# Kernel tuning notes

Hardware: AMD Instinct MI355X
Metric: run time of the kernel (lower is better)

## Reference

```python
import jax, jax.numpy as jnp
import numpy as np

DIM = 512
NUM_HEADS = 8
HEAD_DIM = DIM // NUM_HEADS
SCALE = HEAD_DIM ** -0.5
HIDDEN = int(DIM * 4.0)
LN_EPS = 1e-5


def layer_norm(x, w, b):
    mu = jnp.mean(x, axis=-1, keepdims=True)
    var = jnp.var(x, axis=-1, keepdims=True)
    return (x - mu) * jax.lax.rsqrt(var + LN_EPS) * w + b


def setup_inputs() -> dict:
    key = jax.random.key(0)
    ks = jax.random.split(key, 8)
    s = 0.02
    return {
        "x": jax.random.normal(ks[0], (8, 4096, DIM), dtype=jnp.float32),
        "ln1_w": jnp.ones((DIM,), jnp.float32),
        "ln1_b": jnp.zeros((DIM,), jnp.float32),
        "qkv_w": jax.random.normal(ks[1], (3 * DIM, DIM), jnp.float32) * s,
        "proj_w": jax.random.normal(ks[2], (DIM, DIM), jnp.float32) * s,
        "proj_b": jnp.zeros((DIM,), jnp.float32),
        "ln2_w": jnp.ones((DIM,), jnp.float32),
        "ln2_b": jnp.zeros((DIM,), jnp.float32),
        "fc1_w": jax.random.normal(ks[3], (HIDDEN, DIM), jnp.float32) * s,
        "fc1_b": jnp.zeros((HIDDEN,), jnp.float32),
        "fc2_w": jax.random.normal(ks[4], (DIM, HIDDEN), jnp.float32) * s,
        "fc2_b": jnp.zeros((DIM,), jnp.float32),
        "eca_w": jax.random.normal(ks[5], (1, 1, 3), jnp.float32) * 0.5,
    }


def channel_attention(x, qkv_w, proj_w, proj_b):
    B, N, C = x.shape
    qkv = (x @ qkv_w.T).reshape(B, N, 3, NUM_HEADS, HEAD_DIM)
    qkv = qkv.transpose(2, 0, 3, 1, 4)  # (3, B, h, N, hd)
    q, k, v = qkv[0], qkv[1] * SCALE, qkv[2]
    # cross-covariance attention: (hd x hd) per head
    attn = jax.nn.softmax(jnp.einsum("bhnd,bhne->bhde", k, v), axis=-1)
    out = jnp.einsum("bhde,bhne->bhnd", attn, q)  # (B, h, N, hd)
    out = out.transpose(0, 2, 1, 3).reshape(B, N, C)
    return out @ proj_w.T + proj_b


def mlp_eca(x, fc1_w, fc1_b, fc2_w, fc2_b, eca_w):
    B, N, C = x.shape
    H = W = int(np.sqrt(N))
    h = jax.nn.gelu(x @ fc1_w.T + fc1_b, approximate=False)
    y = h @ fc2_w.T + fc2_b  # (B, N, C)
    # faithful replication of torch .view(B, C, H, W) on contiguous (B, N, C)
    y4 = y.reshape(B, C, H, W)
    pooled = jnp.mean(y4, axis=(2, 3))  # (B, C)
    conv = jax.lax.conv_general_dilated(
        pooled[:, None, :], eca_w, window_strides=(1,), padding=[(1, 1)],
        dimension_numbers=("NCW", "OIW", "NCW"))[:, 0, :]  # (B, C)
    gate = jax.nn.sigmoid(conv)[:, :, None, None]
    y4 = y4 * gate + y4
    return y4.reshape(B, C, H * W).transpose(0, 2, 1)  # (B, N, C)


def reference(x, ln1_w, ln1_b, qkv_w, proj_w, proj_b, ln2_w, ln2_b,
              fc1_w, fc1_b, fc2_w, fc2_b, eca_w):
    cur = layer_norm(x, ln1_w, ln1_b)
    x = x + channel_attention(cur, qkv_w, proj_w, proj_b)
    x = x + mlp_eca(layer_norm(x, ln2_w, ln2_b), fc1_w, fc1_b, fc2_w, fc2_b, eca_w)
    return x
```

## Files before the change

### kernel.cpp

```cpp
#include <hip/hip_runtime.h>
#include <hip/hip_bf16.h>

typedef __bf16 bf16;
typedef __bf16 bf16x8 __attribute__((ext_vector_type(8)));
typedef float floatx4 __attribute__((ext_vector_type(4)));

#define B_    8
#define N_    4096
#define C_    512
#define BN_   32768
#define HID_  2048
#define SCALE_ 0.125f

__device__ __forceinline__ void load_lds16(const void* g, void* l) {
    __builtin_amdgcn_global_load_lds(
        (const __attribute__((address_space(1))) void*)g,
        (__attribute__((address_space(3))) void*)l, 16, 0, 0);
}

__global__ void sniff_kernel(const unsigned int* __restrict__ xw, int* __restrict__ flag)
{
    int t = threadIdx.x;
    int votes = 0;
#pragma unroll
    for (int i = 0; i < 4; i++) {
        unsigned w = xw[t * 4 + i];
        if (w == 0u) continue;
        unsigned a = w & 0xFFFFu;
        unsigned e = (a >> 7) & 0xFFu;
        if (a != 0u && e >= 110u && e <= 135u) votes++; else votes--;
    }
#pragma unroll
    for (int off = 32; off; off >>= 1) votes += __shfl_xor(votes, off);
    __shared__ int s[4];
    if ((t & 63) == 0) s[t >> 6] = votes;
    __syncthreads();
    if (t == 0) *flag = (s[0] + s[1] + s[2] + s[3]) > 0 ? 1 : 0;
}

struct ConvArgs {
    const void* src[12];
    unsigned    dstoff[12];
    int         n[12];
};

__global__ __launch_bounds__(256) void convert_params(
    ConvArgs args, char* __restrict__ ws, const int* __restrict__ flag)
{
    int seg = blockIdx.y;
    int n = args.n[seg];
    int base = blockIdx.x * 2048;
    if (base >= n) return;
    bf16* dst = (bf16*)(ws + args.dstoff[seg]);
    const void* src = args.src[seg];
    bool isbf = (*flag != 0);
#pragma unroll
    for (int j = 0; j < 8; j++) {
        int idx = base + threadIdx.x + j * 256;
        if (idx < n) {
            float v = isbf ? (float)((const bf16*)src)[idx]
                           : ((const float*)src)[idx];
            dst[idx] = (bf16)v;
        }
    }
}

__device__ __forceinline__ void ln_core(float f[8], const bf16* w, const bf16* b,
                                        int lane, bf16* outp)
{
    float s = 0.f, sq = 0.f;
#pragma unroll
    for (int j = 0; j < 8; j++) { s += f[j]; sq += f[j]*f[j]; }
#pragma unroll
    for (int off = 32; off; off >>= 1) { s += __shfl_xor(s, off); sq += __shfl_xor(sq, off); }
    float mean = s * (1.f/512.f);
    float var  = sq * (1.f/512.f) - mean*mean;
    float inv  = rsqrtf(var + 1e-5f);
    bf16x8 wv = *(const bf16x8*)(w + lane*8);
    bf16x8 bv = *(const bf16x8*)(b + lane*8);
    bf16x8 o;
#pragma unroll
    for (int j = 0; j < 8; j++) o[j] = (bf16)((f[j]-mean)*inv*(float)wv[j] + (float)bv[j]);
    *(bf16x8*)outp = o;
}

__global__ __launch_bounds__(256) void ln_dyn_kernel(
    const void* __restrict__ xv, const bf16* __restrict__ w,
    const bf16* __restrict__ b, bf16* __restrict__ out, const int* __restrict__ flag)
{
    int wave = threadIdx.x >> 6, lane = threadIdx.x & 63;
    size_t row = (size_t)blockIdx.x * 4 + wave;
    float f[8];
    if (*flag) {
        bf16x8 v = *(const bf16x8*)((const bf16*)xv + row * C_ + lane * 8);
#pragma unroll
        for (int j = 0; j < 8; j++) f[j] = (float)v[j];
    } else {
        const float4* p = (const float4*)((const float*)xv + row * C_ + lane * 8);
        float4 v0 = p[0], v1 = p[1];
        f[0]=v0.x; f[1]=v0.y; f[2]=v0.z; f[3]=v0.w;
        f[4]=v1.x; f[5]=v1.y; f[6]=v1.z; f[7]=v1.w;
    }
    ln_core(f, w, b, lane, out + row * C_ + lane*8);
}

__global__ __launch_bounds__(256) void ln_b16_kernel(
    const bf16* __restrict__ x, const bf16* __restrict__ w,
    const bf16* __restrict__ b, bf16* __restrict__ out)
{
    int wave = threadIdx.x >> 6, lane = threadIdx.x & 63;
    size_t row = (size_t)blockIdx.x * 4 + wave;
    bf16x8 v = *(const bf16x8*)(x + row * C_ + lane * 8);
    float f[8];
#pragma unroll
    for (int j = 0; j < 8; j++) f[j] = (float)v[j];
    ln_core(f, w, b, lane, out + row * C_ + lane*8);
}

__global__ __launch_bounds__(256) void ln_f32_kernel(
    const float* __restrict__ x, const bf16* __restrict__ w,
    const bf16* __restrict__ b, bf16* __restrict__ out)
{
    int wave = threadIdx.x >> 6, lane = threadIdx.x & 63;
    size_t row = (size_t)blockIdx.x * 4 + wave;
    const float4* p = (const float4*)(x + row * C_ + lane * 8);
    float4 v0 = p[0], v1 = p[1];
    float f[8] = { v0.x, v0.y, v0.z, v0.w, v1.x, v1.y, v1.z, v1.w };
    ln_core(f, w, b, lane, out + row * C_ + lane*8);
}

enum { EPI_NONE = 0, EPI_BIAS = 1, EPI_BIAS_RESID = 2, EPI_BIAS_GELU = 3, EPI_QKV = 4 };

__device__ __forceinline__ void stage_half(
    const bf16* __restrict__ G, int ldk, bf16* lbase, int t)
{
#pragma unroll
    for (int i = 0; i < 2; i++) {
        int c  = i * 512 + t;
        int cp = c ^ (((c >> 5) & 1) << 1);
        load_lds16(G + (size_t)(cp >> 3) * ldk + (cp & 7) * 8, lbase + c * 8);
    }
}

#define PHASE(qq)  {                                                           \
    constexpr int aH = (qq) >> 1, bH = (qq) & 1;                               \
    const bf16* Ab = &Asl[s][aH][0][0];                                        \
    const bf16* Bb = &Bsl[s][bH][0][0];                                        \
    bf16x8 af[4][2], bfv[2][2];                                                \
    _Pragma("unroll") for (int mi = 0; mi < 4; mi++) {                         \
        int row = wm * 64 + mi * 16 + l16;                                     \
        int xo  = ((row >> 2) & 1) << 4;                                       \
        _Pragma("unroll") for (int ks = 0; ks < 2; ks++)                       \
            af[mi][ks] = *(const bf16x8*)(Ab + row * 64 +                      \
                          ((ks * 32 + quad * 8) ^ xo));                        \
    }                                                                          \
    _Pragma("unroll") for (int ni = 0; ni < 2; ni++) {                         \
        int row = wn * 32 + ni * 16 + l16;                                     \
        int xo  = ((row >> 2) & 1) << 4;                                       \
        _Pragma("unroll") for (int ks = 0; ks < 2; ks++)                       \
            bfv[ni][ks] = *(const bf16x8*)(Bb + row * 64 +                     \
                          ((ks * 32 + quad * 8) ^ xo));                        \
    }                                                                          \
    if ((qq) == 0 && kt + 1 < NKT)                                             \
        stage_half(A + (size_t)(m0 + 128) * K + (size_t)(kt + 1) * 64, K,      \
                   &Asl[s ^ 1][1][0][0], t);                                   \
    if ((qq) == 1 && kt + 1 < NKT)                                             \
        stage_half(W + (size_t)(n0 + 128) * K + (size_t)(kt + 1) * 64, K,      \
                   &Bsl[s ^ 1][1][0][0], t);                                   \
    if ((qq) == 2 && kt + 2 < NKT)                                             \
        stage_half(A + (size_t)m0 * K + (size_t)(kt + 2) * 64, K,              \
                   &Asl[s][0][0][0], t);                                       \
    if ((qq) == 3 && kt + 2 < NKT)                                             \
        stage_half(W + (size_t)n0 * K + (size_t)(kt + 2) * 64, K,              \
                   &Bsl[s][0][0][0], t);                                       \
    if ((qq) == 3 && kt + 1 < NKT) {                                           \
        if (kt + 2 < NKT) asm volatile("s_waitcnt vmcnt(4)");                  \
        else              asm volatile("s_waitcnt vmcnt(0)");                  \
    }                                                                          \
    __builtin_amdgcn_s_barrier();                                              \
    asm volatile("s_waitcnt lgkmcnt(0)");                                      \
    __builtin_amdgcn_s_setprio(1);                                             \
    _Pragma("unroll") for (int mi = 0; mi < 4; mi++)                           \
    _Pragma("unroll") for (int ni = 0; ni < 2; ni++)                           \
    _Pragma("unroll") for (int ks = 0; ks < 2; ks++)                           \
        acc[aH * 4 + mi][bH * 2 + ni] = __builtin_amdgcn_mfma_f32_16x16x32_bf16( \
            af[mi][ks], bfv[ni][ks], acc[aH * 4 + mi][bH * 2 + ni], 0, 0, 0);  \
    __builtin_amdgcn_s_setprio(0);                                             \
    __builtin_amdgcn_s_barrier();                                              \
}

template<typename OutT, int EPI>
__global__ __launch_bounds__(512, 2) void gemm256(
    const bf16* __restrict__ A, const bf16* __restrict__ W,
    const bf16* __restrict__ bias, const void* __restrict__ resid,
    const int* __restrict__ flag,
    OutT* __restrict__ Cout, bf16* __restrict__ Cout2, int M, int Nn, int K)
{
    __shared__ bf16 Asl[2][2][128][64];
    __shared__ bf16 Bsl[2][2][128][64];
    const int t = threadIdx.x;
    const int wv = t >> 6, lane = t & 63;
    const int quad = lane >> 4, l16 = lane & 15;
    const int wm = wv >> 2, wn = wv & 3;
    const int Nt = Nn >> 8;
    const int id = blockIdx.x;
    const int xcd = id & 7, j = id >> 3;
    const int m0 = ((j / Nt) * 8 + xcd) * 256;
    const int n0 = (j % Nt) * 256;
    const int NKT = K >> 6;

    floatx4 acc[8][4] = {};

    stage_half(A + (size_t)m0 * K,           K, &Asl[0][0][0][0], t);
    stage_half(W + (size_t)n0 * K,           K, &Bsl[0][0][0][0], t);
    stage_half(A + (size_t)(m0 + 128) * K,   K, &Asl[0][1][0][0], t);
    stage_half(W + (size_t)(n0 + 128) * K,   K, &Bsl[0][1][0][0], t);
    stage_half(A + (size_t)m0 * K + 64,      K, &Asl[1][0][0][0], t);
    stage_half(W + (size_t)n0 * K + 64,      K, &Bsl[1][0][0][0], t);
    asm volatile("s_waitcnt vmcnt(4)");
    __builtin_amdgcn_s_barrier();

    for (int kt = 0; kt < NKT; ++kt) {
        const int s = kt & 1;
        PHASE(0) PHASE(1) PHASE(2) PHASE(3)
    }

    size_t ldc = (size_t)Nn; int csub = 0; bool to2 = false;
    if (EPI == EPI_QKV) {
        if (n0 >= 512) { to2 = true; ldc = 1024; csub = 512; }
        else           { ldc = 512; }
    }
    bool isbf = false;
    if (EPI == EPI_BIAS_RESID) isbf = (*flag != 0);

#pragma unroll
    for (int mg = 0; mg < 8; mg++) {
        int rowg = m0 + (mg >> 2) * 128 + wm * 64 + (mg & 3) * 16 + quad * 4;
#pragma unroll
        for (int ng = 0; ng < 4; ng++) {
            int col = n0 + (ng >> 1) * 128 + wn * 32 + (ng & 1) * 16 + l16;
            float bv = (EPI == EPI_BIAS || EPI == EPI_BIAS_RESID || EPI == EPI_BIAS_GELU)
                       ? (float)bias[col] : 0.f;
#pragma unroll
            for (int r = 0; r < 4; r++) {
                size_t idx = (size_t)(rowg + r) * ldc + (col - csub);
                float v = acc[mg][ng][r] + bv;
                if (EPI == EPI_BIAS_RESID) {
                    float rres = isbf ? (float)((const bf16*)resid)[idx]
                                      : ((const float*)resid)[idx];
                    v += rres;
                }
                if (EPI == EPI_BIAS_GELU)  v = 0.5f * v * (1.f + erff(v * 0.70710678118654752f));
                if (EPI == EPI_QKV && to2) Cout2[idx] = (bf16)v;
                else                       Cout[idx]  = (OutT)v;
            }
        }
    }
}

__global__ __launch_bounds__(256) void attn_logits_mfma(
    const bf16* __restrict__ kv, float* __restrict__ partial)
{
    __shared__ bf16 Kt[64][136];
    __shared__ bf16 Vt[64][136];
    int s = blockIdx.x, bh = blockIdx.y, b = bh >> 3, h = bh & 7;
    int t = threadIdx.x, wave = t >> 6, lane = t & 63;
    int quad = lane >> 4, l16 = lane & 15;
    floatx4 acc[4] = {};
    for (int c = 0; c < 4; c++) {
        int n0 = s * 512 + c * 128;
        {
            int isv = t >> 7;
            int r   = t & 127;
            const bf16* gp = &kv[((size_t)b * N_ + n0 + r) * 1024 + h * 64 + isv * 512];
            bf16x8 rowv[8];
#pragma unroll
            for (int u = 0; u < 8; u++) rowv[u] = *(const bf16x8*)(gp + u * 8);
            bf16 (*dst)[136] = isv ? Vt : Kt;
#pragma unroll
            for (int u = 0; u < 8; u++)
#pragma unroll
                for (int jj = 0; jj < 8; jj++)
                    dst[u * 8 + jj][r] = rowv[u][jj];
        }
        __syncthreads();
#pragma unroll
        for (int ks = 0; ks < 4; ks++) {
            bf16x8 af = *(const bf16x8*)&Kt[wave * 16 + l16][ks * 32 + quad * 8];
#pragma unroll
            for (int ni = 0; ni < 4; ni++) {
                bf16x8 bfv = *(const bf16x8*)&Vt[ni * 16 + l16][ks * 32 + quad * 8];
                acc[ni] = __builtin_amdgcn_mfma_f32_16x16x32_bf16(af, bfv, acc[ni], 0, 0, 0);
            }
        }
        __syncthreads();
    }
    float* p = partial + ((size_t)bh * 8 + s) * 4096;
#pragma unroll
    for (int ni = 0; ni < 4; ni++)
#pragma unroll
        for (int r = 0; r < 4; r++)
            p[(wave * 16 + quad * 4 + r) * 64 + ni * 16 + l16] = acc[ni][r];
}

__global__ __launch_bounds__(256) void attn_softmax_kernel(
    const float* __restrict__ partial, bf16* __restrict__ attnb)
{
    int bh = blockIdx.y;
    int wave = threadIdx.x >> 6, lane = threadIdx.x & 63;
    for (int r = 0; r < 4; r++) {
        int d = blockIdx.x * 16 + wave * 4 + r;
        float v = 0.f;
#pragma unroll
        for (int s = 0; s < 8; s++) v += partial[((size_t)bh*8 + s)*4096 + d*64 + lane];
        v *= SCALE_;
        float m = v;
#pragma unroll
        for (int off = 32; off; off >>= 1) m = fmaxf(m, __shfl_xor(m, off));
        float p = expf(v - m);
        float sum = p;
#pragma unroll
        for (int off = 32; off; off >>= 1) sum += __shfl_xor(sum, off);
        attnb[(size_t)bh*4096 + d*64 + lane] = (bf16)(p / sum);
    }
}

__global__ __launch_bounds__(256) void attn_apply_mfma(
    const bf16* __restrict__ q, const bf16* __restrict__ attnb,
    bf16* __restrict__ outT)
{
    int bh = blockIdx.y, b = bh >> 3, h = bh & 7;
    int t = threadIdx.x, wave = t >> 6, lane = t & 63;
    int quad = lane >> 4, l16 = lane & 15;
    int nbase = blockIdx.x * 256 + wave * 64;
    bf16x8 bfrag[4][2];
#pragma unroll
    for (int di = 0; di < 4; di++)
#pragma unroll
        for (int ks = 0; ks < 2; ks++)
            bfrag[di][ks] = *(const bf16x8*)&attnb[(size_t)bh*4096 + (di*16 + l16)*64 + ks*32 + quad*8];
    floatx4 acc[4][4] = {};
#pragma unroll
    for (int mi = 0; mi < 4; mi++) {
#pragma unroll
        for (int ks = 0; ks < 2; ks++) {
            bf16x8 af = *(const bf16x8*)&q[((size_t)b*N_ + nbase + mi*16 + l16)*512 + h*64 + ks*32 + quad*8];
#pragma unroll
            for (int di = 0; di < 4; di++)
                acc[mi][di] = __builtin_amdgcn_mfma_f32_16x16x32_bf16(af, bfrag[di][ks], acc[mi][di], 0, 0, 0);
        }
    }
#pragma unroll
    for (int mi = 0; mi < 4; mi++)
#pragma unroll
        for (int di = 0; di < 4; di++)
#pragma unroll
            for (int r = 0; r < 4; r++)
                outT[((size_t)b*N_ + nbase + mi*16 + quad*4 + r)*512 + h*64 + di*16 + l16] =
                    (bf16)acc[mi][di][r];
}

__global__ __launch_bounds__(256) void pooled_kernel(
    const bf16* __restrict__ y, float* __restrict__ pooled)
{
    int bc = blockIdx.x;
    const bf16* p = y + (size_t)bc * 4096 + threadIdx.x * 16;
    float s = 0.f;
#pragma unroll
    for (int i = 0; i < 2; i++) {
        bf16x8 v = *(const bf16x8*)(p + i*8);
#pragma unroll
        for (int j = 0; j < 8; j++) s += (float)v[j];
    }
#pragma unroll
    for (int off = 32; off; off >>= 1) s += __shfl_xor(s, off);
    __shared__ float red[4];
    if ((threadIdx.x & 63) == 0) red[threadIdx.x >> 6] = s;
    __syncthreads();
    if (threadIdx.x == 0)
        pooled[bc] = (red[0] + red[1] + red[2] + red[3]) * (1.f/4096.f);
}

__global__ void gate_kernel(const float* __restrict__ pooled,
                            const bf16* __restrict__ eca_w, float* __restrict__ gate1)
{
    int c = threadIdx.x, b = blockIdx.x;
    float w0 = (float)eca_w[0], w1 = (float)eca_w[1], w2 = (float)eca_w[2];
    const float* p = pooled + b * 512;
    float conv = w1 * p[c];
    if (c > 0)   conv += w0 * p[c-1];
    if (c < 511) conv += w2 * p[c+1];
    float g = 1.f / (1.f + expf(-conv));
    gate1[b * 512 + c] = 1.f + g;
}

__global__ __launch_bounds__(256) void final_rmw(
    const bf16* __restrict__ y, const float* __restrict__ gate1,
    float* __restrict__ out)
{
    int b = blockIdx.z, c0 = blockIdx.y * 64, n0 = blockIdx.x * 64;
    __shared__ float ytile[64][65];
    int t = threadIdx.x;
#pragma unroll
    for (int i = 0; i < 2; i++) {
        int chunk = t * 2 + i;
        int ci = chunk >> 3, nj = (chunk & 7) * 8;
        bf16x8 v = *(const bf16x8*)&y[(size_t)b * ((size_t)N_*C_) + (size_t)(c0+ci) * 4096 + n0 + nj];
#pragma unroll
        for (int j = 0; j < 8; j++) ytile[ci][nj+j] = (float)v[j];
    }
    __syncthreads();
    int cc = t & 63, nb = t >> 6;
    float g = gate1[b * 512 + c0 + cc];
    for (int p = 0; p < 16; p++) {
        int nr = p * 4 + nb;
        size_t idx = ((size_t)b * N_ + n0 + nr) * C_ + c0 + cc;
        out[idx] = out[idx] + g * ytile[cc][nr];
    }
}

__global__ __launch_bounds__(256) void final_fresh(
    const bf16* __restrict__ y, const bf16* __restrict__ x2b,
    const float* __restrict__ gate1, float* __restrict__ out)
{
    int b = blockIdx.z, c0 = blockIdx.y * 64, n0 = blockIdx.x * 64;
    __shared__ float ytile[64][65];
    int t = threadIdx.x;
#pragma unroll
    for (int i = 0; i < 2; i++) {
        int chunk = t * 2 + i;
        int ci = chunk >> 3, nj = (chunk & 7) * 8;
        bf16x8 v = *(const bf16x8*)&y[(size_t)b * ((size_t)N_*C_) + (size_t)(c0+ci) * 4096 + n0 + nj];
#pragma unroll
        for (int j = 0; j < 8; j++) ytile[ci][nj+j] = (float)v[j];
    }
    __syncthreads();
    int cc = t & 63, nb = t >> 6;
    float g = gate1[b * 512 + c0 + cc];
    for (int p = 0; p < 16; p++) {
        int nr = p * 4 + nb;
        size_t idx = ((size_t)b * N_ + n0 + nr) * C_ + c0 + cc;
        out[idx] = (float)x2b[idx] + g * ytile[cc][nr];
    }
}

extern "C" void kernel_launch(void* const* d_in, const int* in_sizes, int n_in,
                              void* d_out, int out_size, void* d_ws, size_t ws_size,
                              hipStream_t stream)
{
    float* outf = (float*)d_out;
    bf16*  outb = (bf16*)d_out;
    char* ws = (char*)d_ws;

    int*   flag    = (int*)ws;
    float* pooled  = (float*)(ws + 4096);
    float* gate1   = (float*)(ws + 20480);
    bf16* ln1_w = (bf16*)(ws + 65536);
    bf16* ln1_b = (bf16*)(ws + 67584);
    bf16* ln2_w = (bf16*)(ws + 69632);
    bf16* ln2_b = (bf16*)(ws + 71680);
    bf16* proj_b= (bf16*)(ws + 73728);
    bf16* fc2_b = (bf16*)(ws + 75776);
    bf16* eca_w = (bf16*)(ws + 77824);
    bf16* fc1_b = (bf16*)(ws + 81920);
    bf16* qkv_w = (bf16*)(ws + ((size_t)1 << 20));
    bf16* proj_w= (bf16*)(ws + (size_t)2621440);
    bf16* fc1_w = (bf16*)(ws + ((size_t)3 << 20));
    bf16* fc2_w = (bf16*)(ws + ((size_t)5 << 20));
    float* partial = (float*)(ws + ((size_t)7  << 20));
    bf16*  attnb   = (bf16*)(ws + ((size_t)15 << 20));
    bf16*  T1      = (bf16*)(ws + ((size_t)16 << 20));
    bf16*  kvbuf   = (bf16*)(ws + ((size_t)48 << 20));
    bf16*  hbuf    = kvbuf;
    bf16*  x2b     = (bf16*)(ws + ((size_t)176 << 20));

    const bool fat = ws_size >= ((size_t)212 << 20);

    sniff_kernel<<<1, 256, 0, stream>>>((const unsigned int*)d_in[0], flag);

    ConvArgs ca;
    const int   srcidx[12] = { 1, 2, 6, 7, 5, 11, 12, 9, 3, 4, 8, 10 };
    const unsigned offs[12] = { 65536, 67584, 69632, 71680, 73728, 75776, 77824, 81920,
                                1u<<20, 2621440u, 3u<<20, 5u<<20 };
    for (int i = 0; i < 12; i++) {
        ca.src[i] = d_in[srcidx[i]];
        ca.dstoff[i] = offs[i];
        ca.n[i] = in_sizes[srcidx[i]];
    }
    convert_params<<<dim3(512, 12), 256, 0, stream>>>(ca, ws, flag);

    ln_dyn_kernel<<<BN_/4, 256, 0, stream>>>(d_in[0], ln1_w, ln1_b, T1, flag);

    gemm256<bf16, EPI_QKV><<<768, 512, 0, stream>>>(
        T1, qkv_w, nullptr, nullptr, flag, outb, kvbuf, BN_, 1536, 512);

    attn_logits_mfma<<<dim3(8, 64), 256, 0, stream>>>(kvbuf, partial);
    attn_softmax_kernel<<<dim3(4, 64), 256, 0, stream>>>(partial, attnb);
    attn_apply_mfma<<<dim3(16, 64), 256, 0, stream>>>(outb, attnb, T1);

    if (fat) {
        gemm256<bf16, EPI_BIAS_RESID><<<256, 512, 0, stream>>>(
            T1, proj_w, proj_b, d_in[0], flag, x2b, nullptr, BN_, 512, 512);
        ln_b16_kernel<<<BN_/4, 256, 0, stream>>>(x2b, ln2_w, ln2_b, T1);
        gemm256<bf16, EPI_BIAS_GELU><<<1024, 512, 0, stream>>>(
            T1, fc1_w, fc1_b, nullptr, flag, hbuf, nullptr, BN_, 2048, 512);
        gemm256<bf16, EPI_BIAS><<<256, 512, 0, stream>>>(
            hbuf, fc2_w, fc2_b, nullptr, flag, T1, nullptr, BN_, 512, 2048);
        pooled_kernel<<<4096, 256, 0, stream>>>(T1, pooled);
        gate_kernel<<<8, 512, 0, stream>>>(pooled, eca_w, gate1);
        final_fresh<<<dim3(64, 8, 8), 256, 0, stream>>>(T1, x2b, gate1, outf);
    } else {
        gemm256<float, EPI_BIAS_RESID><<<256, 512, 0, stream>>>(
            T1, proj_w, proj_b, d_in[0], flag, outf, nullptr, BN_, 512, 512);
        ln_f32_kernel<<<BN_/4, 256, 0, stream>>>(outf, ln2_w, ln2_b, T1);
        for (int ch = 0; ch < 2; ch++) {
            bf16* Tch = T1 + (size_t)ch * 16384 * 512;
            gemm256<bf16, EPI_BIAS_GELU><<<512, 512, 0, stream>>>(
                Tch, fc1_w, fc1_b, nullptr, flag, hbuf, nullptr, 16384, 2048, 512);
            gemm256<bf16, EPI_BIAS><<<128, 512, 0, stream>>>(
                hbuf, fc2_w, fc2_b, nullptr, flag, Tch, nullptr, 16384, 512, 2048);
        }
        pooled_kernel<<<4096, 256, 0, stream>>>(T1, pooled);
        gate_kernel<<<8, 512, 0, stream>>>(pooled, eca_w, gate1);
        final_rmw<<<dim3(64, 8, 8), 256, 0, stream>>>(T1, gate1, outf);
    }
}
```

Baseline: 608.2 us.

## Reorder GEMM quadrants to reuse fragments and use full 8-way LDS swizzle

Changes the LDS swizzle in the 256x256 GEMM from a 1-bit XOR to a full 3-bit XOR on the row index, so the 16-byte fragment reads spread across all banks. It also reorders the four MFMA quadrants (00, 01, 11, 10) so A and B register fragments carry over between phases. This cuts LDS reads per k-tile from four A and four B loads to two of each. The cost is more live fragment registers (af, bf0, bf1) under a 512-thread, 2-blocks-per-CU launch bound, which could cause register spills.

```diff
diff --git a/kernel.cpp b/kernel.cpp
--- a/kernel.cpp
+++ b/kernel.cpp
@@ -137,57 +137,37 @@
 #pragma unroll
     for (int i = 0; i < 2; i++) {
         int c  = i * 512 + t;
-        int cp = c ^ (((c >> 5) & 1) << 1);
-        load_lds16(G + (size_t)(cp >> 3) * ldk + (cp & 7) * 8, lbase + c * 8);
-    }
-}
-
-#define PHASE(qq)  {                                                           \
-    constexpr int aH = (qq) >> 1, bH = (qq) & 1;                               \
-    const bf16* Ab = &Asl[s][aH][0][0];                                        \
-    const bf16* Bb = &Bsl[s][bH][0][0];                                        \
-    bf16x8 af[4][2], bfv[2][2];                                                \
+        int r  = c >> 3;
+        int ls = (c & 7) ^ (r & 7);
+        load_lds16(G + (size_t)r * ldk + ls * 8, lbase + c * 8);
+    }
+}
+
+#define LOAD_AF(half)                                                          \
     _Pragma("unroll") for (int mi = 0; mi < 4; mi++) {                         \
         int row = wm * 64 + mi * 16 + l16;                                     \
-        int xo  = ((row >> 2) & 1) << 4;                                       \
         _Pragma("unroll") for (int ks = 0; ks < 2; ks++)                       \
-            af[mi][ks] = *(const bf16x8*)(Ab + row * 64 +                      \
-                          ((ks * 32 + quad * 8) ^ xo));                        \
-    }                                                                          \
+            af[mi][ks] = *(const bf16x8*)(&Asl[s][half][0][0] + row * 64 +     \
+                ((ks * 32 + quad * 8) ^ ((row & 7) << 3)));                    \
+    }
+#define LOAD_BF(dst, half)                                                     \
     _Pragma("unroll") for (int ni = 0; ni < 2; ni++) {                         \
         int row = wn * 32 + ni * 16 + l16;                                     \
-        int xo  = ((row >> 2) & 1) << 4;                                       \
         _Pragma("unroll") for (int ks = 0; ks < 2; ks++)                       \
-            bfv[ni][ks] = *(const bf16x8*)(Bb + row * 64 +                     \
-                          ((ks * 32 + quad * 8) ^ xo));                        \
-    }                                                                          \
-    if ((qq) == 0 && kt + 1 < NKT)                                             \
-        stage_half(A + (size_t)(m0 + 128) * K + (size_t)(kt + 1) * 64, K,      \
-                   &Asl[s ^ 1][1][0][0], t);                                   \
-    if ((qq) == 1 && kt + 1 < NKT)                                             \
-        stage_half(W + (size_t)(n0 + 128) * K + (size_t)(kt + 1) * 64, K,      \
-                   &Bsl[s ^ 1][1][0][0], t);                                   \
-    if ((qq) == 2 && kt + 2 < NKT)                                             \
-        stage_half(A + (size_t)m0 * K + (size_t)(kt + 2) * 64, K,              \
-                   &Asl[s][0][0][0], t);                                       \
-    if ((qq) == 3 && kt + 2 < NKT)                                             \
-        stage_half(W + (size_t)n0 * K + (size_t)(kt + 2) * 64, K,              \
-                   &Bsl[s][0][0][0], t);                                       \
-    if ((qq) == 3 && kt + 1 < NKT) {                                           \
-        if (kt + 2 < NKT) asm volatile("s_waitcnt vmcnt(4)");                  \
-        else              asm volatile("s_waitcnt vmcnt(0)");                  \
-    }                                                                          \
+            dst[ni][ks] = *(const bf16x8*)(&Bsl[s][half][0][0] + row * 64 +    \
+                ((ks * 32 + quad * 8) ^ ((row & 7) << 3)));                    \
+    }
+#define MFMA_Q(AH, BH, BFR)                                                    \
     __builtin_amdgcn_s_barrier();                                              \
     asm volatile("s_waitcnt lgkmcnt(0)");                                      \
     __builtin_amdgcn_s_setprio(1);                                             \
     _Pragma("unroll") for (int mi = 0; mi < 4; mi++)                           \
     _Pragma("unroll") for (int ni = 0; ni < 2; ni++)                           \
     _Pragma("unroll") for (int ks = 0; ks < 2; ks++)                           \
-        acc[aH * 4 + mi][bH * 2 + ni] = __builtin_amdgcn_mfma_f32_16x16x32_bf16( \
-            af[mi][ks], bfv[ni][ks], acc[aH * 4 + mi][bH * 2 + ni], 0, 0, 0);  \
+        acc[(AH)*4+mi][(BH)*2+ni] = __builtin_amdgcn_mfma_f32_16x16x32_bf16(   \
+            af[mi][ks], BFR[ni][ks], acc[(AH)*4+mi][(BH)*2+ni], 0, 0, 0);      \
     __builtin_amdgcn_s_setprio(0);                                             \
-    __builtin_amdgcn_s_barrier();                                              \
-}
+    __builtin_amdgcn_s_barrier();
 
 template<typename OutT, int EPI>
 __global__ __launch_bounds__(512, 2) void gemm256(
@@ -210,6 +190,7 @@
     const int NKT = K >> 6;
 
     floatx4 acc[8][4] = {};
+    bf16x8 af[4][2], bf0[2][2], bf1[2][2];
 
     stage_half(A + (size_t)m0 * K,           K, &Asl[0][0][0][0], t);
     stage_half(W + (size_t)n0 * K,           K, &Bsl[0][0][0][0], t);
@@ -222,7 +203,30 @@
 
     for (int kt = 0; kt < NKT; ++kt) {
         const int s = kt & 1;
-        PHASE(0) PHASE(1) PHASE(2) PHASE(3)
+        LOAD_AF(0)
+        LOAD_BF(bf0, 0)
+        if (kt + 1 < NKT)
+            stage_half(A + (size_t)(m0 + 128) * K + (size_t)(kt + 1) * 64, K,
+                       &Asl[s ^ 1][1][0][0], t);
+        MFMA_Q(0, 0, bf0)
+        LOAD_BF(bf1, 1)
+        if (kt + 1 < NKT)
+            stage_half(W + (size_t)(n0 + 128) * K + (size_t)(kt + 1) * 64, K,
+                       &Bsl[s ^ 1][1][0][0], t);
+        MFMA_Q(0, 1, bf1)
+        LOAD_AF(1)
+        if (kt + 2 < NKT)
+            stage_half(A + (size_t)m0 * K + (size_t)(kt + 2) * 64, K,
+                       &Asl[s][0][0][0], t);
+        MFMA_Q(1, 1, bf1)
+        if (kt + 2 < NKT)
+            stage_half(W + (size_t)n0 * K + (size_t)(kt + 2) * 64, K,
+                       &Bsl[s][0][0][0], t);
+        if (kt + 1 < NKT) {
+            if (kt + 2 < NKT) asm volatile("s_waitcnt vmcnt(4)");
+            else              asm volatile("s_waitcnt vmcnt(0)");
+        }
+        MFMA_Q(1, 0, bf0)
     }
 
     size_t ldc = (size_t)Nn; int csub = 0; bool to2 = false;
```

After: 549.9 us. 9.6% less time.
